# Performance work log

Measured on AMD Instinct MI355X. Metric: run time of the kernel, lower is better.

## Reference

```python
import jax, jax.numpy as jnp
import numpy as np

N_NODES = 50000
N_EDGES = 400000
N_GROUPS = 10000
N_GRAPHS = 256
IN_CH = 64
EDGE_DIM = 16
HID = 64
HEADS = 4
OUT_CH = 1


def segment_mean(vals, idx, n):
    s = jax.ops.segment_sum(vals, idx, num_segments=n)
    c = jax.ops.segment_sum(jnp.ones(idx.shape[0], vals.dtype), idx, num_segments=n)
    c = jnp.maximum(c, 1.0).reshape((n,) + (1,) * (vals.ndim - 1))
    return s / c


def gatv2(x, src, dst, wl, wr, att, bias, edge_attr=None, we=None):
    # PyG GATv2Conv (concat=True, negative_slope=0.2, add_self_loops=True,
    # fill_value='mean', share_weights=False).
    N = x.shape[0]
    H, C = att.shape
    loop = jnp.arange(N, dtype=src.dtype)
    s = jnp.concatenate([src, loop])
    d = jnp.concatenate([dst, loop])
    dc = jnp.minimum(d, N - 1)  # clamp dummy (masked) targets for gathers
    xl = (x @ wl).reshape(N, H, C)  # source transform
    xr = (x @ wr).reshape(N, H, C)  # target transform
    m = xl[s] + xr[dc]  # [E+N, H, C]
    if edge_attr is not None:
        loop_attr = segment_mean(edge_attr, dst, N)  # self-loop attr = mean of incoming
        e = jnp.concatenate([edge_attr, loop_attr], axis=0) @ we
        m = m + e.reshape(-1, H, C)
    score = jnp.sum(jax.nn.leaky_relu(m, 0.2) * att, axis=-1)  # [E+N, H]
    smax = jax.ops.segment_max(score, d, num_segments=N)
    ex = jnp.exp(score - smax[dc])
    den = jax.ops.segment_sum(ex, d, num_segments=N)
    alpha = ex / den[dc]
    out = jax.ops.segment_sum(alpha[..., None] * xl[s], d, num_segments=N)
    return out.reshape(N, H * C) + bias


def setup_inputs() -> dict:
    key = jax.random.key(0)
    ks = jax.random.split(key, 32)
    p = lambda i, shape: jax.random.normal(ks[i], shape, jnp.float32) * 0.05
    x = jax.random.normal(ks[0], (N_NODES, IN_CH), jnp.float32)
    edge_index = jax.random.randint(ks[1], (2, N_EDGES), 0, N_NODES)
    edge_attr = jax.random.normal(ks[2], (N_EDGES, EDGE_DIM), jnp.float32)
    batch = (jnp.arange(N_NODES) * N_GRAPHS) // N_NODES
    pharma_index = (jnp.arange(N_NODES) * N_GROUPS) // N_NODES
    return dict(
        x=x, edge_index=edge_index, edge_attr=edge_attr, batch=batch,
        pharma_index=pharma_index, num_graphs=N_GRAPHS,
        w_edge=p(3, (EDGE_DIM, HID)), b_edge=jnp.zeros((HID,), jnp.float32),
        g1_wl=p(4, (IN_CH, HEADS * HID)), g1_wr=p(5, (IN_CH, HEADS * HID)),
        g1_att=p(6, (HEADS, HID)), g1_we=p(7, (HID, HEADS * HID)),
        g1_b=jnp.zeros((HEADS * HID,), jnp.float32),
        g2_wl=p(8, (HEADS * HID, HID)), g2_wr=p(9, (HEADS * HID, HID)),
        g2_att=p(10, (1, HID)), g2_we=p(11, (HID, HID)),
        g2_b=jnp.zeros((HID,), jnp.float32),
        g3_wl=p(12, (HID, HID)), g3_wr=p(13, (HID, HID)),
        g3_att=p(14, (1, HID)), g3_b=jnp.zeros((HID,), jnp.float32),
        g4_wl=p(15, (HID, HID)), g4_wr=p(16, (HID, HID)),
        g4_att=p(17, (1, HID)), g4_b=jnp.zeros((HID,), jnp.float32),
        w1=p(18, (HID, 64)), b1=jnp.zeros((64,), jnp.float32),
        w2=p(19, (64, OUT_CH)), b2=jnp.zeros((OUT_CH,), jnp.float32),
    )


def reference(x, edge_index, edge_attr, batch, pharma_index, num_graphs,
              w_edge, b_edge,
              g1_wl, g1_wr, g1_att, g1_we, g1_b,
              g2_wl, g2_wr, g2_att, g2_we, g2_b,
              g3_wl, g3_wr, g3_att, g3_b,
              g4_wl, g4_wr, g4_att, g4_b,
              w1, b1, w2, b2):
    src, dst = edge_index[0], edge_index[1]
    ea = edge_attr @ w_edge + b_edge  # edge_embed
    h = jax.nn.elu(gatv2(x, src, dst, g1_wl, g1_wr, g1_att, g1_b, ea, g1_we))
    h = jax.nn.elu(gatv2(h, src, dst, g2_wl, g2_wr, g2_att, g2_b, ea, g2_we))
    # pharmacophore pooling (scatter_mean)
    gx = segment_mean(h, pharma_index, N_GROUPS)
    rbatch = segment_mean(batch.astype(jnp.float32), pharma_index, N_GROUPS).astype(jnp.int32)
    # reduced-graph edges: map node edges to group indices, drop intra-group
    # self-edges by routing their target to a dummy segment N_GROUPS.
    sg = pharma_index[src]
    dg = pharma_index[dst]
    dg = jnp.where(sg != dg, dg, N_GROUPS)
    h = jax.nn.elu(gatv2(gx, sg, dg, g3_wl, g3_wr, g3_att, g3_b))
    h = jax.nn.elu(gatv2(h, sg, dg, g4_wl, g4_wr, g4_att, g4_b))
    h = segment_mean(h, rbatch, num_graphs)  # global_mean_pool
    h = jax.nn.relu(h @ w1 + b1)
    return h @ w2 + b2
```

## Files before the change

### kernel.cpp

```cpp
#include <hip/hip_runtime.h>
#include <cstdint>
#include <cstddef>

#define NN 50000
#define NE 400000
#define NG 10000
#define NBG 256

#define LOG2E 1.4426950408889634f

__device__ __forceinline__ int rfl(int v) { return __builtin_amdgcn_readfirstlane(v); }

template <int CTRL>
__device__ __forceinline__ float dpp_mov(float v) {
  return __int_as_float(__builtin_amdgcn_update_dpp(0, __float_as_int(v), CTRL, 0xf, 0xf, true));
}
__device__ __forceinline__ float wave_sum_dpp(float v) {
  v += dpp_mov<0x111>(v);
  v += dpp_mov<0x112>(v);
  v += dpp_mov<0x114>(v);
  v += dpp_mov<0x118>(v);
  v += dpp_mov<0x142>(v);
  v += dpp_mov<0x143>(v);
  return __int_as_float(__builtin_amdgcn_readlane(__float_as_int(v), 63));
}


__global__ void count_dst_kernel(const int* __restrict__ dst, int* __restrict__ cnt, int E) {
  int e = blockIdx.x * blockDim.x + threadIdx.x;
  if (e < E) atomicAdd(&cnt[dst[e]], 1);
}

__global__ void fill_node_kernel(const int* __restrict__ src, const int* __restrict__ dst,
                                 int* __restrict__ cursor, int2* __restrict__ cpack, int E) {
  int e = blockIdx.x * blockDim.x + threadIdx.x;
  if (e < E) {
    int pos = atomicAdd(&cursor[dst[e]], 1);
    cpack[pos] = make_int2(src[e], e);
  }
}

__global__ void count_grp_kernel(const int* __restrict__ src, const int* __restrict__ dst,
                                 const int* __restrict__ ph, int* __restrict__ cnt, int E) {
  int e = blockIdx.x * blockDim.x + threadIdx.x;
  if (e < E) {
    int sg = ph[src[e]], dg = ph[dst[e]];
    if (sg != dg) atomicAdd(&cnt[dg], 1);
  }
}

__global__ void fill_grp_kernel(const int* __restrict__ src, const int* __restrict__ dst,
                                const int* __restrict__ ph, int* __restrict__ cursor,
                                int* __restrict__ gsrc, int E) {
  int e = blockIdx.x * blockDim.x + threadIdx.x;
  if (e < E) {
    int sg = ph[src[e]], dg = ph[dst[e]];
    if (sg != dg) {
      int pos = atomicAdd(&cursor[dg], 1);
      gsrc[pos] = sg;
    }
  }
}

__global__ void exscan_block_kernel(const int* __restrict__ cnt, int* __restrict__ rowptr, int n) {
  __shared__ int wsum[16];
  int tid = threadIdx.x;
  int chunk = (n + 1023) >> 10;
  int s0 = tid * chunk;
  int s1 = s0 + chunk; if (s1 > n) s1 = n;
  int sum = 0;
  for (int i = s0; i < s1; i++) sum += cnt[i];
  int lane = tid & 63, w = tid >> 6;
  int v = sum, s = sum;
#pragma unroll
  for (int off = 1; off < 64; off <<= 1) {
    int t = __shfl_up(s, off);
    if (lane >= off) s += t;
  }
  if (lane == 63) wsum[w] = s;
  __syncthreads();
  if (tid == 0) {
    int c = 0;
#pragma unroll
    for (int i = 0; i < 16; i++) { int t = wsum[i]; wsum[i] = c; c += t; }
  }
  __syncthreads();
  int run = wsum[w] + (s - v);
  for (int i = s0; i < s1; i++) { rowptr[i] = run; run += cnt[i]; }
  if (tid == 1023) rowptr[n] = run;
}


__global__ void mean_attr_kernel(const int* __restrict__ rowptr, const int2* __restrict__ cpack,
                                 const float* __restrict__ eattr, float* __restrict__ mattr, int N) {
  int n = blockIdx.x * blockDim.x + threadIdx.x;
  if (n >= N) return;
  int e0 = rowptr[n], e1 = rowptr[n + 1];
  float s[16];
#pragma unroll
  for (int k = 0; k < 16; k++) s[k] = 0.f;
  for (int p = e0; p < e1; p++) {
    const float4* ep = (const float4*)(eattr + (size_t)cpack[p].y * 16);
#pragma unroll
    for (int q = 0; q < 4; q++) {
      float4 a = ep[q];
      s[q * 4 + 0] += a.x; s[q * 4 + 1] += a.y; s[q * 4 + 2] += a.z; s[q * 4 + 3] += a.w;
    }
  }
  float inv = (e1 > e0) ? 1.f / (float)(e1 - e0) : 0.f;
  float4* mp = (float4*)(mattr + (size_t)n * 16);
#pragma unroll
  for (int q = 0; q < 4; q++) {
    float4 a;
    a.x = s[q * 4 + 0] * inv; a.y = s[q * 4 + 1] * inv;
    a.z = s[q * 4 + 2] * inv; a.w = s[q * 4 + 3] * inv;
    mp[q] = a;
  }
}

__global__ void fuse_we_kernel(const float* __restrict__ w_edge, const float* __restrict__ b_edge,
                               const float* __restrict__ g1_we, const float* __restrict__ g2_we,
                               float* __restrict__ We2_1, float* __restrict__ be2_1,
                               float* __restrict__ We2_2, float* __restrict__ be2_2) {
  int t = blockIdx.x * blockDim.x + threadIdx.x;
  if (t < 16 * 256) {
    int k = t >> 8, j = t & 255;
    float s = 0.f;
    for (int c = 0; c < 64; c++) s += w_edge[k * 64 + c] * g1_we[c * 256 + j];
    We2_1[t] = s;
  } else if (t < 16 * 256 + 256) {
    int j = t - 16 * 256;
    float s = 0.f;
    for (int c = 0; c < 64; c++) s += b_edge[c] * g1_we[c * 256 + j];
    be2_1[j] = s;
  } else if (t < 16 * 256 + 256 + 16 * 64) {
    int u = t - (16 * 256 + 256);
    int k = u >> 6, j = u & 63;
    float s = 0.f;
    for (int c = 0; c < 64; c++) s += w_edge[k * 64 + c] * g2_we[c * 64 + j];
    We2_2[u] = s;
  } else if (t < 16 * 256 + 256 + 16 * 64 + 64) {
    int j = t - (16 * 256 + 256 + 16 * 64);
    float s = 0.f;
    for (int c = 0; c < 64; c++) s += b_edge[c] * g2_we[c * 64 + j];
    be2_2[j] = s;
  }
}

template <int IN, int OUT>
__global__ __launch_bounds__(256) void matvec_kernel(int nRows,
    const float* __restrict__ X, const float* __restrict__ W, float* __restrict__ Y) {
  constexpr int KT = IN / 64;
  const int lane = threadIdx.x & 63;
  const int wv = threadIdx.x >> 6;
  const int row = (blockIdx.x * 4 + wv) * 64 + lane;
  const int rc = row < nRows ? row : nRows - 1;
  const int jc = blockIdx.y;
  const float* xp = X + (size_t)rc * IN;
  float acc[64];
#pragma unroll
  for (int j = 0; j < 64; j++) acc[j] = 0.f;
  for (int kt = 0; kt < KT; kt++) {
    float xt[64];
#pragma unroll
    for (int q = 0; q < 16; q++) {
      const float4 v = *(const float4*)(xp + kt * 64 + q * 4);
      xt[q * 4 + 0] = v.x; xt[q * 4 + 1] = v.y; xt[q * 4 + 2] = v.z; xt[q * 4 + 3] = v.w;
    }
    const float* wb = W + (size_t)kt * 64 * OUT + jc * 64;
#pragma unroll
    for (int k = 0; k < 64; k++) {
#pragma unroll
      for (int j = 0; j < 64; j++) acc[j] += xt[k] * wb[(size_t)k * OUT + j];
    }
  }
  if (row < nRows) {
    float* yp = Y + (size_t)row * OUT + jc * 64;
#pragma unroll
    for (int q = 0; q < 16; q++) {
      float4 v;
      v.x = acc[q * 4 + 0]; v.y = acc[q * 4 + 1]; v.z = acc[q * 4 + 2]; v.w = acc[q * 4 + 3];
      *(float4*)(yp + q * 4) = v;
    }
  }
}


#define GAT_LOADE(pos, SUF)                                                     \
  do {                                                                          \
    int s_;                                                                     \
    if constexpr (HASE) {                                                       \
      int2 se_ = cpack[pos];                                                    \
      s_ = rfl(se_.x);                                                          \
      const int eid_ = rfl(se_.y);                                              \
      const float4* ep_ = (const float4*)(eattr + (size_t)eid_ * 16);           \
      float4 q0_ = ep_[0], q1_ = ep_[1], q2_ = ep_[2], q3_ = ep_[3];            \
      ea##SUF[0]  = q0_.x; ea##SUF[1]  = q0_.y; ea##SUF[2]  = q0_.z; ea##SUF[3]  = q0_.w; \
      ea##SUF[4]  = q1_.x; ea##SUF[5]  = q1_.y; ea##SUF[6]  = q1_.z; ea##SUF[7]  = q1_.w; \
      ea##SUF[8]  = q2_.x; ea##SUF[9]  = q2_.y; ea##SUF[10] = q2_.z; ea##SUF[11] = q2_.w; \
      ea##SUF[12] = q3_.x; ea##SUF[13] = q3_.y; ea##SUF[14] = q3_.z; ea##SUF[15] = q3_.w; \
    } else {                                                                    \
      s_ = rfl(csrc[pos]);                                                      \
    }                                                                           \
    const float* xp_ = xl + (size_t)s_ * F + lane;                              \
    _Pragma("unroll")                                                           \
    for (int h_ = 0; h_ < H; h_++) xs##SUF[h_] = xp_[h_ * 64];                  \
  } while (0)

#define GAT_COMPUTE(SUF)                                                        \
  do {                                                                          \
    float ev_[H], sc_[H];                                                       \
    _Pragma("unroll")                                                           \
    for (int h_ = 0; h_ < H; h_++) ev_[h_] = HASE ? be2_r[h_] : 0.f;            \
    if constexpr (HASE) {                                                       \
      _Pragma("unroll")                                                         \
      for (int k_ = 0; k_ < 16; k_++) {                                         \
        _Pragma("unroll")                                                       \
        for (int h_ = 0; h_ < H; h_++) ev_[h_] += ea##SUF[k_] * wreg[k_ * H + h_]; \
      }                                                                         \
    }                                                                           \
    _Pragma("unroll")                                                           \
    for (int h_ = 0; h_ < H; h_++) {                                            \
      float v_ = xs##SUF[h_] + xr_r[h_] + ev_[h_];                              \
      v_ = fmaxf(v_, 0.f) + 0.2f * fminf(v_, 0.f);                              \
      sc_[h_] = wave_sum_dpp(v_ * att_r[h_]);                                   \
    }                                                                           \
    _Pragma("unroll")                                                           \
    for (int h_ = 0; h_ < H; h_++) {                                            \
      float ex_ = exp2f(sc_[h_]);                                               \
      den[h_] += ex_;                                                           \
      acc[h_] += ex_ * xs##SUF[h_];                                             \
    }                                                                           \
  } while (0)

template <int H, bool HASE>
__global__ __launch_bounds__(256) void gat_kernel(
    int N,
    const int* __restrict__ rowptr,
    const int2* __restrict__ cpack,
    const int* __restrict__ csrc,
    const float* __restrict__ eattr,
    const float* __restrict__ mattr,
    const float* __restrict__ We2,
    const float* __restrict__ be2,
    const float* __restrict__ xl,
    const float* __restrict__ xr,
    const float* __restrict__ att,
    const float* __restrict__ bias,
    float* __restrict__ out)
{
  constexpr int F = H * 64;
  const int lane = threadIdx.x & 63;
  const int wv = threadIdx.x >> 6;

  float att_r[H], bias_r[H], be2_r[H], wreg[16 * H];
#pragma unroll
  for (int h = 0; h < H; h++) {
    att_r[h] = att[h * 64 + lane] * LOG2E;
    bias_r[h] = bias[h * 64 + lane];
    be2_r[h] = 0.f;
  }
  if constexpr (HASE) {
#pragma unroll
    for (int h = 0; h < H; h++) be2_r[h] = be2[h * 64 + lane];
#pragma unroll
    for (int k = 0; k < 16; k++)
#pragma unroll
      for (int h = 0; h < H; h++) wreg[k * H + h] = We2[k * F + h * 64 + lane];
  }

  const int wave_id = blockIdx.x * 4 + wv;
  const int wstride = gridDim.x * 4;
  for (int n0 = wave_id; n0 < N; n0 += wstride) {
    const int n = rfl(n0);
    const int e0 = rfl(rowptr[n]);
    const int e1 = rfl(rowptr[n + 1]);
    const int nE = e1 - e0;
    float xr_r[H], xls[H];
    {
      const float* xpr = xr + (size_t)n * F + lane;
      const float* xpl = xl + (size_t)n * F + lane;
#pragma unroll
      for (int h = 0; h < H; h++) { xr_r[h] = xpr[h * 64]; xls[h] = xpl[h * 64]; }
    }

    float den[H], acc[H];
    {
      float ev[H];
#pragma unroll
      for (int h = 0; h < H; h++) ev[h] = 0.f;
      if constexpr (HASE) {
        if (nE > 0) {
          const float4* mp4 = (const float4*)(mattr + (size_t)n * 16);
          float ma[16];
#pragma unroll
          for (int q = 0; q < 4; q++) {
            float4 a = mp4[q];
            ma[q * 4 + 0] = a.x; ma[q * 4 + 1] = a.y; ma[q * 4 + 2] = a.z; ma[q * 4 + 3] = a.w;
          }
#pragma unroll
          for (int k = 0; k < 16; k++)
#pragma unroll
            for (int h = 0; h < H; h++) ev[h] += ma[k] * wreg[k * H + h];
#pragma unroll
          for (int h = 0; h < H; h++) ev[h] += be2_r[h];
        }
      }
#pragma unroll
      for (int h = 0; h < H; h++) {
        float v = xls[h] + xr_r[h] + ev[h];
        v = fmaxf(v, 0.f) + 0.2f * fminf(v, 0.f);
        float ex = exp2f(wave_sum_dpp(v * att_r[h]));
        den[h] = ex; acc[h] = ex * xls[h];
      }
    }

    if constexpr (!HASE && H == 1) {
      float xsA[1], xsB[1], xsC[1], xsD[1];
      float eaA[1], eaB[1], eaC[1], eaD[1];
      (void)eaA; (void)eaB; (void)eaC; (void)eaD;
      if (nE > 0) GAT_LOADE(e0 + 0, A);
      if (nE > 1) GAT_LOADE(e0 + 1, B);
      if (nE > 2) GAT_LOADE(e0 + 2, C);
      if (nE > 3) GAT_LOADE(e0 + 3, D);
      int i = 0;
      for (; i + 7 < nE; i += 4) {
        GAT_COMPUTE(A); GAT_LOADE(e0 + i + 4, A);
        GAT_COMPUTE(B); GAT_LOADE(e0 + i + 5, B);
        GAT_COMPUTE(C); GAT_LOADE(e0 + i + 6, C);
        GAT_COMPUTE(D); GAT_LOADE(e0 + i + 7, D);
      }
      int rem = nE - i;
      if (rem > 0) { GAT_COMPUTE(A); if (rem > 4) GAT_LOADE(e0 + i + 4, A); }
      if (rem > 1) { GAT_COMPUTE(B); if (rem > 5) GAT_LOADE(e0 + i + 5, B); }
      if (rem > 2) { GAT_COMPUTE(C); if (rem > 6) GAT_LOADE(e0 + i + 6, C); }
      if (rem > 3) GAT_COMPUTE(D);
      if (rem > 4) GAT_COMPUTE(A);
      if (rem > 5) GAT_COMPUTE(B);
      if (rem > 6) GAT_COMPUTE(C);
    } else {
      float xsA[H], xsB[H];
      float eaA[16], eaB[16];
      (void)eaA; (void)eaB;
      if (nE > 0) GAT_LOADE(e0, A);
      if (nE > 1) GAT_LOADE(e0 + 1, B);
      int i = 0;
      for (; i + 3 < nE; i += 2) {
        GAT_COMPUTE(A);
        GAT_LOADE(e0 + i + 2, A);
        GAT_COMPUTE(B);
        GAT_LOADE(e0 + i + 3, B);
      }
      if (i < nE) {
        GAT_COMPUTE(A);
        if (i + 2 < nE) GAT_LOADE(e0 + i + 2, A);
      }
      if (i + 1 < nE) GAT_COMPUTE(B);
      if (i + 2 < nE) GAT_COMPUTE(A);
    }

#pragma unroll
    for (int h = 0; h < H; h++) {
      float o = acc[h] / den[h] + bias_r[h];
      out[(size_t)n * F + h * 64 + lane] = o > 0.f ? o : (__expf(o) - 1.f);
    }
  }
}


__global__ void pool_ph_scatter_kernel(const float* __restrict__ h, const int* __restrict__ ph,
                                       const int* __restrict__ batch, float* __restrict__ gsum,
                                       float* __restrict__ bsum, int* __restrict__ gcnt, int N) {
  int t = blockIdx.x * blockDim.x + threadIdx.x;
  if (t >= N * 64) return;
  int n = t >> 6, c = t & 63;
  int g = ph[n];
  atomicAdd(&gsum[(size_t)g * 64 + c], h[t]);
  if (c == 0) {
    atomicAdd(&gcnt[g], 1);
    atomicAdd(&bsum[g], (float)batch[n]);
  }
}

__global__ void pool_ph_final_kernel(const float* __restrict__ gsum, const float* __restrict__ bsum,
                                     const int* __restrict__ gcnt, float* __restrict__ gx,
                                     int* __restrict__ rbatch, int G) {
  int t = blockIdx.x * blockDim.x + threadIdx.x;
  if (t >= G * 64) return;
  int g = t >> 6, c = t & 63;
  float cn = fmaxf((float)gcnt[g], 1.f);
  gx[t] = gsum[t] / cn;
  if (c == 0) rbatch[g] = (int)(bsum[g] / cn);
}

__global__ void pool_graph_scatter_kernel(const float* __restrict__ h, const int* __restrict__ rbatch,
                                          float* __restrict__ psum, int* __restrict__ pcnt, int G) {
  int t = blockIdx.x * blockDim.x + threadIdx.x;
  if (t >= G * 64) return;
  int g = t >> 6, c = t & 63;
  int b = rbatch[g];
  atomicAdd(&psum[(size_t)b * 64 + c], h[t]);
  if (c == 0) atomicAdd(&pcnt[b], 1);
}

__global__ void pool_graph_final_kernel(const float* __restrict__ psum, const int* __restrict__ pcnt,
                                        float* __restrict__ pooled) {
  int t = blockIdx.x * blockDim.x + threadIdx.x;
  if (t >= NBG * 64) return;
  int b = t >> 6;
  pooled[t] = psum[t] / fmaxf((float)pcnt[b], 1.f);
}


__global__ void fc1_kernel(const float* __restrict__ pooled, const float* __restrict__ w1,
                           const float* __restrict__ b1, float* __restrict__ o) {
  int g = blockIdx.x, lane = threadIdx.x;
  float p = pooled[g * 64 + lane];
  float acc = b1[lane];
#pragma unroll 8
  for (int k = 0; k < 64; k++) acc += __shfl(p, k, 64) * w1[k * 64 + lane];
  o[g * 64 + lane] = fmaxf(acc, 0.f);
}

__global__ void fc2_kernel(const float* __restrict__ o1, const float* __restrict__ w2,
                           const float* __restrict__ b2, float* __restrict__ out) {
  int g = threadIdx.x;
  float acc = b2[0];
  for (int k = 0; k < 64; k++) acc += o1[g * 64 + k] * w2[k];
  out[g] = acc;
}


extern "C" void kernel_launch(void* const* d_in, const int* in_sizes, int n_in,
                              void* d_out, int out_size, void* d_ws, size_t ws_size,
                              hipStream_t stream) {
  (void)in_sizes; (void)n_in; (void)out_size; (void)ws_size;
  const float* x      = (const float*)d_in[0];
  const int*   eidx   = (const int*)d_in[1];
  const float* eattr  = (const float*)d_in[2];
  const int*   batch  = (const int*)d_in[3];
  const int*   ph     = (const int*)d_in[4];
  const float* w_edge = (const float*)d_in[6];
  const float* b_edge = (const float*)d_in[7];
  const float* g1_wl  = (const float*)d_in[8];
  const float* g1_wr  = (const float*)d_in[9];
  const float* g1_att = (const float*)d_in[10];
  const float* g1_we  = (const float*)d_in[11];
  const float* g1_b   = (const float*)d_in[12];
  const float* g2_wl  = (const float*)d_in[13];
  const float* g2_wr  = (const float*)d_in[14];
  const float* g2_att = (const float*)d_in[15];
  const float* g2_we  = (const float*)d_in[16];
  const float* g2_b   = (const float*)d_in[17];
  const float* g3_wl  = (const float*)d_in[18];
  const float* g3_wr  = (const float*)d_in[19];
  const float* g3_att = (const float*)d_in[20];
  const float* g3_b   = (const float*)d_in[21];
  const float* g4_wl  = (const float*)d_in[22];
  const float* g4_wr  = (const float*)d_in[23];
  const float* g4_att = (const float*)d_in[24];
  const float* g4_b   = (const float*)d_in[25];
  const float* w1     = (const float*)d_in[26];
  const float* b1     = (const float*)d_in[27];
  const float* w2     = (const float*)d_in[28];
  const float* b2     = (const float*)d_in[29];
  float* out = (float*)d_out;
  const int* src = eidx;
  const int* dst = eidx + NE;

  char* ws = (char*)d_ws;
  size_t off = 0;
  auto alloc = [&](size_t bytes) -> void* {
    size_t o = off;
    off = (off + bytes + 255) & ~(size_t)255;
    return (void*)(ws + o);
  };
  int*   rowptr  = (int*)alloc((NN + 1) * 4);
  int*   cursor  = (int*)alloc((NN + 1) * 4);
  int2*  cpack   = (int2*)alloc((size_t)NE * 8);
  int*   growptr = (int*)alloc((NG + 1) * 4);
  int*   gcursor = (int*)alloc((NG + 1) * 4);
  int*   gsrc    = (int*)alloc((size_t)NE * 4);
  float* mattr   = (float*)alloc((size_t)NN * 16 * 4);
  float* We2_1   = (float*)alloc(16 * 256 * 4);
  float* be2_1   = (float*)alloc(256 * 4);
  float* We2_2   = (float*)alloc(16 * 64 * 4);
  float* be2_2   = (float*)alloc(64 * 4);
  float* xl1     = (float*)alloc((size_t)NN * 256 * 4);
  float* xr1     = (float*)alloc((size_t)NN * 256 * 4);
  float* h1      = (float*)alloc((size_t)NN * 256 * 4);
  float* bsum    = (float*)alloc(NG * 4);
  int*   gcnt    = (int*)alloc(NG * 4);
  int*   rbatch  = (int*)alloc(NG * 4);
  float* psum    = (float*)alloc(NBG * 64 * 4);
  int*   pcnt    = (int*)alloc(NBG * 4);
  float* pooled  = (float*)alloc(NBG * 64 * 4);
  float* fc1o    = (float*)alloc(NBG * 64 * 4);
  float* xl2 = xl1;
  float* xr2 = xl1 + (size_t)NN * 64;
  float* h2  = xl1 + (size_t)NN * 128;
  float* gsum = xr1;
  float* gx   = xr1 + (size_t)NG * 64 * 1;
  float* xl3  = xr1 + (size_t)NG * 64 * 2;
  float* xr3  = xr1 + (size_t)NG * 64 * 3;
  float* h3   = xr1 + (size_t)NG * 64 * 4;
  float* xl4  = xr1 + (size_t)NG * 64 * 5;
  float* xr4  = xr1 + (size_t)NG * 64 * 6;
  float* h4   = xr1 + (size_t)NG * 64 * 7;

  hipMemsetAsync(cursor, 0, (NN + 1) * 4, stream);
  count_dst_kernel<<<(NE + 255) / 256, 256, 0, stream>>>(dst, cursor, NE);
  exscan_block_kernel<<<1, 1024, 0, stream>>>(cursor, rowptr, NN);
  hipMemcpyAsync(cursor, rowptr, (NN + 1) * 4, hipMemcpyDeviceToDevice, stream);
  fill_node_kernel<<<(NE + 255) / 256, 256, 0, stream>>>(src, dst, cursor, cpack, NE);
  mean_attr_kernel<<<(NN + 255) / 256, 256, 0, stream>>>(rowptr, cpack, eattr, mattr, NN);
  fuse_we_kernel<<<(16 * 256 + 256 + 16 * 64 + 64 + 255) / 256, 256, 0, stream>>>(
      w_edge, b_edge, g1_we, g2_we, We2_1, be2_1, We2_2, be2_2);

  {
    dim3 g1((NN + 255) / 256, 4);
    matvec_kernel<64, 256><<<g1, 256, 0, stream>>>(NN, x, g1_wl, xl1);
    matvec_kernel<64, 256><<<g1, 256, 0, stream>>>(NN, x, g1_wr, xr1);
  }
  gat_kernel<4, true><<<(NN + 3) / 4, 256, 0, stream>>>(NN, rowptr, cpack, nullptr, eattr, mattr,
                                                        We2_1, be2_1, xl1, xr1, g1_att, g1_b, h1);
  {
    dim3 g2((NN + 255) / 256, 1);
    matvec_kernel<256, 64><<<g2, 256, 0, stream>>>(NN, h1, g2_wl, xl2);
    matvec_kernel<256, 64><<<g2, 256, 0, stream>>>(NN, h1, g2_wr, xr2);
  }
  gat_kernel<1, true><<<(NN + 3) / 4, 256, 0, stream>>>(NN, rowptr, cpack, nullptr, eattr, mattr,
                                                        We2_2, be2_2, xl2, xr2, g2_att, g2_b, h2);

  hipMemsetAsync(gsum, 0, (size_t)NG * 64 * 4, stream);
  hipMemsetAsync(bsum, 0, NG * 4, stream);
  hipMemsetAsync(gcnt, 0, NG * 4, stream);
  pool_ph_scatter_kernel<<<(NN * 64 + 255) / 256, 256, 0, stream>>>(h2, ph, batch, gsum, bsum, gcnt, NN);
  pool_ph_final_kernel<<<(NG * 64 + 255) / 256, 256, 0, stream>>>(gsum, bsum, gcnt, gx, rbatch, NG);

  hipMemsetAsync(gcursor, 0, (NG + 1) * 4, stream);
  count_grp_kernel<<<(NE + 255) / 256, 256, 0, stream>>>(src, dst, ph, gcursor, NE);
  exscan_block_kernel<<<1, 1024, 0, stream>>>(gcursor, growptr, NG);
  hipMemcpyAsync(gcursor, growptr, (NG + 1) * 4, hipMemcpyDeviceToDevice, stream);
  fill_grp_kernel<<<(NE + 255) / 256, 256, 0, stream>>>(src, dst, ph, gcursor, gsrc, NE);

  {
    dim3 g3((NG + 255) / 256, 1);
    matvec_kernel<64, 64><<<g3, 256, 0, stream>>>(NG, gx, g3_wl, xl3);
    matvec_kernel<64, 64><<<g3, 256, 0, stream>>>(NG, gx, g3_wr, xr3);
    gat_kernel<1, false><<<(NG + 3) / 4, 256, 0, stream>>>(NG, growptr, nullptr, gsrc, nullptr,
                                                           nullptr, nullptr, nullptr, xl3, xr3,
                                                           g3_att, g3_b, h3);
    matvec_kernel<64, 64><<<g3, 256, 0, stream>>>(NG, h3, g4_wl, xl4);
    matvec_kernel<64, 64><<<g3, 256, 0, stream>>>(NG, h3, g4_wr, xr4);
    gat_kernel<1, false><<<(NG + 3) / 4, 256, 0, stream>>>(NG, growptr, nullptr, gsrc, nullptr,
                                                           nullptr, nullptr, nullptr, xl4, xr4,
                                                           g4_att, g4_b, h4);
  }

  hipMemsetAsync(psum, 0, NBG * 64 * 4, stream);
  hipMemsetAsync(pcnt, 0, NBG * 4, stream);
  pool_graph_scatter_kernel<<<(NG * 64 + 255) / 256, 256, 0, stream>>>(h4, rbatch, psum, pcnt, NG);
  pool_graph_final_kernel<<<(NBG * 64 + 255) / 256, 256, 0, stream>>>(psum, pcnt, pooled);
  fc1_kernel<<<NBG, 64, 0, stream>>>(pooled, w1, b1, fc1o);
  fc2_kernel<<<1, 256, 0, stream>>>(fc1o, w2, b2, out);
}
```

Before: 1.218 ms.

## Interleave head layout for layer-1 features, merge memsets, cap GAT grids

Adds a transposing matvec that writes the layer-1 xl/xr in head-interleaved order, so each GAT lane gathers all four heads with one float4 load instead of four strided scalar loads. Leaky-ReLU is rewritten as 0.6*m + 0.4*|m| with pre-scaled attention weights. The exscan kernel now also writes the cursor copy, which removes the device-to-device memcpys. Several memsets are merged by packing their buffers contiguously, and the GAT grids are capped at 2048 blocks on the assumption that the kernel loops over nodes with a grid stride. The cost is extra LDS traffic for the transpose and a reliance on that grid-stride loop being present.

After: 1.481 ms. 1.22x slower.

```diff
diff --git a/kernel.cpp b/kernel.cpp
--- a/kernel.cpp
+++ b/kernel.cpp
@@ -8,6 +8,8 @@
 #define NBG 256
 
 #define LOG2E 1.4426950408889634f
+
+static inline int imin(int a, int b) { return a < b ? a : b; }
 
 __device__ __forceinline__ int rfl(int v) { return __builtin_amdgcn_readfirstlane(v); }
 
@@ -62,7 +64,8 @@
   }
 }
 
-__global__ void exscan_block_kernel(const int* __restrict__ cnt, int* __restrict__ rowptr, int n) {
+__global__ void exscan_block_kernel(const int* __restrict__ cnt, int* __restrict__ rowptr,
+                                    int* __restrict__ cursor_out, int n) {
   __shared__ int wsum[16];
   int tid = threadIdx.x;
   int chunk = (n + 1023) >> 10;
@@ -86,7 +89,12 @@
   }
   __syncthreads();
   int run = wsum[w] + (s - v);
-  for (int i = s0; i < s1; i++) { rowptr[i] = run; run += cnt[i]; }
+  for (int i = s0; i < s1; i++) {
+    int c = cnt[i];
+    rowptr[i] = run;
+    cursor_out[i] = run;
+    run += c;
+  }
   if (tid == 1023) rowptr[n] = run;
 }
 
@@ -185,6 +193,46 @@
   }
 }
 
+__global__ __launch_bounds__(256) void matvec_tr_kernel(int nRows,
+    const float* __restrict__ X, const float* __restrict__ W, float* __restrict__ Y) {
+  __shared__ float tile[64 * 257];
+  const int lane = threadIdx.x & 63;
+  const int h = threadIdx.x >> 6;
+  const int rb = blockIdx.x * 64;
+  const int row = rb + lane;
+  const int rc = row < nRows ? row : nRows - 1;
+  const float* xp = X + (size_t)rc * 64;
+  float xt[64];
+#pragma unroll
+  for (int q = 0; q < 16; q++) {
+    const float4 v = *(const float4*)(xp + q * 4);
+    xt[q * 4 + 0] = v.x; xt[q * 4 + 1] = v.y; xt[q * 4 + 2] = v.z; xt[q * 4 + 3] = v.w;
+  }
+  float acc[64];
+#pragma unroll
+  for (int j = 0; j < 64; j++) acc[j] = 0.f;
+  const float* wb = W + h * 64;
+#pragma unroll
+  for (int k = 0; k < 64; k++) {
+#pragma unroll
+    for (int j = 0; j < 64; j++) acc[j] += xt[k] * wb[(size_t)k * 256 + j];
+  }
+#pragma unroll
+  for (int j = 0; j < 64; j++) tile[lane * 257 + j * 4 + h] = acc[j];
+  __syncthreads();
+  const int r = threadIdx.x >> 2, q = threadIdx.x & 3;
+  if (rb + r < nRows) {
+    float4* yp = (float4*)(Y + (size_t)(rb + r) * 256 + q * 64);
+    const float* tp = tile + r * 257 + q * 64;
+#pragma unroll
+    for (int i = 0; i < 16; i++) {
+      float4 v;
+      v.x = tp[i * 4 + 0]; v.y = tp[i * 4 + 1]; v.z = tp[i * 4 + 2]; v.w = tp[i * 4 + 3];
+      yp[i] = v;
+    }
+  }
+}
+
 
 #define GAT_LOADE(pos, SUF)                                                     \
   do {                                                                          \
@@ -202,9 +250,12 @@
     } else {                                                                    \
       s_ = rfl(csrc[pos]);                                                      \
     }                                                                           \
-    const float* xp_ = xl + (size_t)s_ * F + lane;                              \
-    _Pragma("unroll")                                                           \
-    for (int h_ = 0; h_ < H; h_++) xs##SUF[h_] = xp_[h_ * 64];                  \
+    if constexpr (H == 4) {                                                     \
+      float4 v_ = ((const float4*)xl)[(size_t)s_ * 64 + lane];                  \
+      xs##SUF[0] = v_.x; xs##SUF[1] = v_.y; xs##SUF[2] = v_.z; xs##SUF[3] = v_.w; \
+    } else {                                                                    \
+      xs##SUF[0] = xl[(size_t)s_ * 64 + lane];                                  \
+    }                                                                           \
   } while (0)
 
 #define GAT_COMPUTE(SUF)                                                        \
@@ -221,9 +272,8 @@
     }                                                                           \
     _Pragma("unroll")                                                           \
     for (int h_ = 0; h_ < H; h_++) {                                            \
-      float v_ = xs##SUF[h_] + xr_r[h_] + ev_[h_];                              \
-      v_ = fmaxf(v_, 0.f) + 0.2f * fminf(v_, 0.f);                              \
-      sc_[h_] = wave_sum_dpp(v_ * att_r[h_]);                                   \
+      float m_ = xs##SUF[h_] + xr_r[h_] + ev_[h_];                              \
+      sc_[h_] = wave_sum_dpp(m_ * att06_r[h_] + fabsf(m_) * att04_r[h_]);       \
     }                                                                           \
     _Pragma("unroll")                                                           \
     for (int h_ = 0; h_ < H; h_++) {                                            \
@@ -253,10 +303,12 @@
   const int lane = threadIdx.x & 63;
   const int wv = threadIdx.x >> 6;
 
-  float att_r[H], bias_r[H], be2_r[H], wreg[16 * H];
+  float att06_r[H], att04_r[H], bias_r[H], be2_r[H], wreg[16 * H];
 #pragma unroll
   for (int h = 0; h < H; h++) {
-    att_r[h] = att[h * 64 + lane] * LOG2E;
+    float a = att[h * 64 + lane] * LOG2E;
+    att06_r[h] = 0.6f * a;
+    att04_r[h] = 0.4f * a;
     bias_r[h] = bias[h * 64 + lane];
     be2_r[h] = 0.f;
   }
@@ -277,11 +329,14 @@
     const int e1 = rfl(rowptr[n + 1]);
     const int nE = e1 - e0;
     float xr_r[H], xls[H];
-    {
-      const float* xpr = xr + (size_t)n * F + lane;
-      const float* xpl = xl + (size_t)n * F + lane;
-#pragma unroll
-      for (int h = 0; h < H; h++) { xr_r[h] = xpr[h * 64]; xls[h] = xpl[h * 64]; }
+    if constexpr (H == 4) {
+      float4 a = ((const float4*)xr)[(size_t)n * 64 + lane];
+      xr_r[0] = a.x; xr_r[1] = a.y; xr_r[2] = a.z; xr_r[3] = a.w;
+      float4 b = ((const float4*)xl)[(size_t)n * 64 + lane];
+      xls[0] = b.x; xls[1] = b.y; xls[2] = b.z; xls[3] = b.w;
+    } else {
+      xr_r[0] = xr[(size_t)n * 64 + lane];
+      xls[0] = xl[(size_t)n * 64 + lane];
     }
 
     float den[H], acc[H];
@@ -308,9 +363,8 @@
       }
 #pragma unroll
       for (int h = 0; h < H; h++) {
-        float v = xls[h] + xr_r[h] + ev[h];
-        v = fmaxf(v, 0.f) + 0.2f * fminf(v, 0.f);
-        float ex = exp2f(wave_sum_dpp(v * att_r[h]));
+        float m = xls[h] + xr_r[h] + ev[h];
+        float ex = exp2f(wave_sum_dpp(m * att06_r[h] + fabsf(m) * att04_r[h]));
         den[h] = ex; acc[h] = ex * xls[h];
       }
     }
@@ -489,77 +543,72 @@
   float* xl1     = (float*)alloc((size_t)NN * 256 * 4);
   float* xr1     = (float*)alloc((size_t)NN * 256 * 4);
   float* h1      = (float*)alloc((size_t)NN * 256 * 4);
-  float* bsum    = (float*)alloc(NG * 4);
-  int*   gcnt    = (int*)alloc(NG * 4);
   int*   rbatch  = (int*)alloc(NG * 4);
-  float* psum    = (float*)alloc(NBG * 64 * 4);
-  int*   pcnt    = (int*)alloc(NBG * 4);
+  float* psum    = (float*)alloc((size_t)NBG * 65 * 4);
+  int*   pcnt    = (int*)(psum + (size_t)NBG * 64);
   float* pooled  = (float*)alloc(NBG * 64 * 4);
   float* fc1o    = (float*)alloc(NBG * 64 * 4);
   float* xl2 = xl1;
   float* xr2 = xl1 + (size_t)NN * 64;
   float* h2  = xl1 + (size_t)NN * 128;
   float* gsum = xr1;
-  float* gx   = xr1 + (size_t)NG * 64 * 1;
-  float* xl3  = xr1 + (size_t)NG * 64 * 2;
-  float* xr3  = xr1 + (size_t)NG * 64 * 3;
-  float* h3   = xr1 + (size_t)NG * 64 * 4;
-  float* xl4  = xr1 + (size_t)NG * 64 * 5;
-  float* xr4  = xr1 + (size_t)NG * 64 * 6;
-  float* h4   = xr1 + (size_t)NG * 64 * 7;
+  float* bsum = xr1 + (size_t)NG * 64;
+  int*   gcnt = (int*)(xr1 + (size_t)NG * 65);
+  float* gx   = xr1 + (size_t)NG * 66;
+  float* xl3  = gx  + (size_t)NG * 64;
+  float* xr3  = xl3 + (size_t)NG * 64;
+  float* h3   = xr3 + (size_t)NG * 64;
+  float* xl4  = h3  + (size_t)NG * 64;
+  float* xr4  = xl4 + (size_t)NG * 64;
+  float* h4   = xr4 + (size_t)NG * 64;
 
   hipMemsetAsync(cursor, 0, (NN + 1) * 4, stream);
   count_dst_kernel<<<(NE + 255) / 256, 256, 0, stream>>>(dst, cursor, NE);
-  exscan_block_kernel<<<1, 1024, 0, stream>>>(cursor, rowptr, NN);
-  hipMemcpyAsync(cursor, rowptr, (NN + 1) * 4, hipMemcpyDeviceToDevice, stream);
+  exscan_block_kernel<<<1, 1024, 0, stream>>>(cursor, rowptr, cursor, NN);
   fill_node_kernel<<<(NE + 255) / 256, 256, 0, stream>>>(src, dst, cursor, cpack, NE);
   mean_attr_kernel<<<(NN + 255) / 256, 256, 0, stream>>>(rowptr, cpack, eattr, mattr, NN);
   fuse_we_kernel<<<(16 * 256 + 256 + 16 * 64 + 64 + 255) / 256, 256, 0, stream>>>(
       w_edge, b_edge, g1_we, g2_we, We2_1, be2_1, We2_2, be2_2);
 
   {
-    dim3 g1((NN + 255) / 256, 4);
-    matvec_kernel<64, 256><<<g1, 256, 0, stream>>>(NN, x, g1_wl, xl1);
-    matvec_kernel<64, 256><<<g1, 256, 0, stream>>>(NN, x, g1_wr, xr1);
-  }
-  gat_kernel<4, true><<<(NN + 3) / 4, 256, 0, stream>>>(NN, rowptr, cpack, nullptr, eattr, mattr,
-                                                        We2_1, be2_1, xl1, xr1, g1_att, g1_b, h1);
+    int g1 = (NN + 63) / 64;
+    matvec_tr_kernel<<<g1, 256, 0, stream>>>(NN, x, g1_wl, xl1);
+    matvec_tr_kernel<<<g1, 256, 0, stream>>>(NN, x, g1_wr, xr1);
+  }
+  gat_kernel<4, true><<<2048, 256, 0, stream>>>(NN, rowptr, cpack, nullptr, eattr, mattr,
+                                                We2_1, be2_1, xl1, xr1, g1_att, g1_b, h1);
   {
     dim3 g2((NN + 255) / 256, 1);
     matvec_kernel<256, 64><<<g2, 256, 0, stream>>>(NN, h1, g2_wl, xl2);
     matvec_kernel<256, 64><<<g2, 256, 0, stream>>>(NN, h1, g2_wr, xr2);
   }
-  gat_kernel<1, true><<<(NN + 3) / 4, 256, 0, stream>>>(NN, rowptr, cpack, nullptr, eattr, mattr,
-                                                        We2_2, be2_2, xl2, xr2, g2_att, g2_b, h2);
-
-  hipMemsetAsync(gsum, 0, (size_t)NG * 64 * 4, stream);
-  hipMemsetAsync(bsum, 0, NG * 4, stream);
-  hipMemsetAsync(gcnt, 0, NG * 4, stream);
+  gat_kernel<1, true><<<2048, 256, 0, stream>>>(NN, rowptr, cpack, nullptr, eattr, mattr,
+                                                We2_2, be2_2, xl2, xr2, g2_att, g2_b, h2);
+
+  hipMemsetAsync(xr1, 0, (size_t)NG * 66 * 4, stream);
   pool_ph_scatter_kernel<<<(NN * 64 + 255) / 256, 256, 0, stream>>>(h2, ph, batch, gsum, bsum, gcnt, NN);
   pool_ph_final_kernel<<<(NG * 64 + 255) / 256, 256, 0, stream>>>(gsum, bsum, gcnt, gx, rbatch, NG);
 
   hipMemsetAsync(gcursor, 0, (NG + 1) * 4, stream);
   count_grp_kernel<<<(NE + 255) / 256, 256, 0, stream>>>(src, dst, ph, gcursor, NE);
-  exscan_block_kernel<<<1, 1024, 0, stream>>>(gcursor, growptr, NG);
-  hipMemcpyAsync(gcursor, growptr, (NG + 1) * 4, hipMemcpyDeviceToDevice, stream);
+  exscan_block_kernel<<<1, 1024, 0, stream>>>(gcursor, growptr, gcursor, NG);
   fill_grp_kernel<<<(NE + 255) / 256, 256, 0, stream>>>(src, dst, ph, gcursor, gsrc, NE);
 
   {
     dim3 g3((NG + 255) / 256, 1);
     matvec_kernel<64, 64><<<g3, 256, 0, stream>>>(NG, gx, g3_wl, xl3);
     matvec_kernel<64, 64><<<g3, 256, 0, stream>>>(NG, gx, g3_wr, xr3);
-    gat_kernel<1, false><<<(NG + 3) / 4, 256, 0, stream>>>(NG, growptr, nullptr, gsrc, nullptr,
-                                                           nullptr, nullptr, nullptr, xl3, xr3,
-                                                           g3_att, g3_b, h3);
+    gat_kernel<1, false><<<imin((NG + 3) / 4, 2048), 256, 0, stream>>>(
+        NG, growptr, nullptr, gsrc, nullptr, nullptr, nullptr, nullptr,
+        xl3, xr3, g3_att, g3_b, h3);
     matvec_kernel<64, 64><<<g3, 256, 0, stream>>>(NG, h3, g4_wl, xl4);
     matvec_kernel<64, 64><<<g3, 256, 0, stream>>>(NG, h3, g4_wr, xr4);
-    gat_kernel<1, false><<<(NG + 3) / 4, 256, 0, stream>>>(NG, growptr, nullptr, gsrc, nullptr,
-                                                           nullptr, nullptr, nullptr, xl4, xr4,
-                                                           g4_att, g4_b, h4);
-  }
-
-  hipMemsetAsync(psum, 0, NBG * 64 * 4, stream);
-  hipMemsetAsync(pcnt, 0, NBG * 4, stream);
+    gat_kernel<1, false><<<imin((NG + 3) / 4, 2048), 256, 0, stream>>>(
+        NG, growptr, nullptr, gsrc, nullptr, nullptr, nullptr, nullptr,
+        xl4, xr4, g4_att, g4_b, h4);
+  }
+
+  hipMemsetAsync(psum, 0, (size_t)NBG * 65 * 4, stream);
   pool_graph_scatter_kernel<<<(NG * 64 + 255) / 256, 256, 0, stream>>>(h4, rbatch, psum, pcnt, NG);
   pool_graph_final_kernel<<<(NBG * 64 + 255) / 256, 256, 0, stream>>>(psum, pcnt, pooled);
   fc1_kernel<<<NBG, 64, 0, stream>>>(pooled, w1, b1, fc1o);
```
